# Optimization experiments

Measured on AMD Instinct MI355X. Metric: run time of the kernel, lower is better.

Reference implementation:

```python
import jax, jax.numpy as jnp
import numpy as np

NUM_EXPERTS = 8
DIM = 2048
BATCH = 8192


def setup_inputs() -> dict:
    key = jax.random.key(0)
    k_x, k_ids, k_w, k_b = jax.random.split(key, 4)
    x = jax.random.normal(k_x, (BATCH, DIM), dtype=jnp.float32)
    cam_pred_ids = jax.random.randint(k_ids, (BATCH,), 0, NUM_EXPERTS, dtype=jnp.int64)
    # torch nn.Linear default init: U(-1/sqrt(in), 1/sqrt(in)); W is [out, in]
    bound = 1.0 / np.sqrt(DIM)
    W = jax.random.uniform(k_w, (NUM_EXPERTS, DIM, DIM), dtype=jnp.float32,
                           minval=-bound, maxval=bound)
    b = jax.random.uniform(k_b, (NUM_EXPERTS, DIM), dtype=jnp.float32,
                           minval=-bound, maxval=bound)
    return {"x": x, "cam_pred_ids": cam_pred_ids, "W": W, "b": b}


def reference(x, cam_pred_ids, W, b):
    # Per-sample expert routing: out[i] = x[i] + relu(x[i] @ W[e].T + b[e]),
    # where e = cam_pred_ids[i]. Vectorized as 8 full-batch GEMMs with masked
    # combine (fixed small expert count -> Python loop is structural, not data).
    h = jnp.zeros_like(x)
    for e in range(NUM_EXPERTS):
        he = jax.nn.relu(x @ W[e].T + b[e])          # [B, D]
        mask = (cam_pred_ids == e)[:, None]
        h = h + jnp.where(mask, he, jnp.zeros((), dtype=x.dtype))
    return x + h
```

## Files before the change

### kernel.cpp

```cpp
#include <hip/hip_runtime.h>
#include <hip/hip_bf16.h>
#include <stdint.h>

#define BATCH 8192
#define DIM   2048
#define NEXP  8
#define BM    128
#define BN    128
#define BK    32
#define NITER (DIM / BK)
#define MAX_TILES 72
#define NBLK  (DIM / BN)
#define NROWS 9216
#define NCVTB 4096

typedef __bf16 bf16x8 __attribute__((ext_vector_type(8)));
typedef float  f32x4  __attribute__((ext_vector_type(4)));

#define XG_BYTE_OFF 40960ull
#define WB_BYTE_OFF 37789696ull
#define WS_NEED     104898560ull

#define AS1(p) ((const __attribute__((address_space(1))) void*)(p))
#define AS3(p) ((__attribute__((address_space(3))) void*)(p))

__device__ __forceinline__ unsigned f2bf2(float lo, float hi) {
    unsigned ul = __float_as_uint(lo), uh = __float_as_uint(hi);
    ul = (ul + 0x7FFFu + ((ul >> 16) & 1u)) >> 16;
    uh = (uh + 0x7FFFu + ((uh >> 16) & 1u)) >> 16;
    return (uh << 16) | ul;
}

__global__ void k_plan(const int* __restrict__ ids, int* __restrict__ ws,
                       int* __restrict__ rowmap) {
    __shared__ int sc[256 * NEXP];
    __shared__ int seg[NEXP];
    __shared__ int tot[NEXP];
    int t = threadIdx.x;
#pragma unroll
    for (int e = 0; e < NEXP; e++) sc[t * NEXP + e] = 0;
    int base = t * 32;
    for (int i = 0; i < 32; i++) sc[t * NEXP + ids[base + i]]++;
    __syncthreads();
    if (t < NEXP) {
        int run = 0;
        for (int j = 0; j < 256; j++) {
            int v = sc[j * NEXP + t];
            sc[j * NEXP + t] = run;
            run += v;
        }
        tot[t] = run;
    }
    __syncthreads();
    if (t == 0) {
        int pos = 0, mt = 0;
        for (int e = 0; e < NEXP; e++) {
            int c = tot[e];
            seg[e]     = pos;
            ws[e]      = c;
            ws[32 + e] = pos;
            int ntl = (c + BM - 1) / BM;
            for (int tt = 0; tt < ntl; tt++) {
                ws[64  + mt] = e;
                ws[160 + mt] = pos + tt * BM;
                int v = c - tt * BM;
                ws[256 + mt] = v < BM ? v : BM;
                mt++;
            }
            pos += ntl * BM;
        }
        ws[48] = mt;
        ws[49] = pos;
    }
    __syncthreads();
    for (int i = t; i < NROWS; i += 256) rowmap[i] = -1;
    __syncthreads();
    for (int i = 0; i < 32; i++) {
        int e = ids[base + i];
        int p = seg[e] + sc[t * NEXP + e]++;
        rowmap[p] = base + i;
    }
}

__global__ void k_prep(const float* __restrict__ x,
                       const int* __restrict__ rowmap,
                       unsigned short* __restrict__ xg,
                       const float4* __restrict__ W, uint4* __restrict__ Wb) {
    int b = blockIdx.x;
    int t = threadIdx.x;
    if (b >= NROWS) {
        size_t base = (size_t)(b - NROWS) * 1024;
#pragma unroll
        for (int j = 0; j < 4; j++) {
            size_t o = base + (size_t)j * 256 + t;
            float4 a = W[o * 2], c = W[o * 2 + 1];
            uint4 v;
            v.x = f2bf2(a.x, a.y);  v.y = f2bf2(a.z, a.w);
            v.z = f2bf2(c.x, c.y);  v.w = f2bf2(c.z, c.w);
            Wb[o] = v;
        }
        return;
    }
    int orig = rowmap[b];
    uint4* o = (uint4*)(xg + (size_t)b * DIM);
    if (orig < 0) {
        o[t] = make_uint4(0, 0, 0, 0);
        return;
    }
    const float4* xr = (const float4*)(x + (size_t)orig * DIM);
    float4 a = xr[t * 2], b4 = xr[t * 2 + 1];
    uint4 v;
    v.x = f2bf2(a.x, a.y);   v.y = f2bf2(a.z, a.w);
    v.z = f2bf2(b4.x, b4.y); v.w = f2bf2(b4.z, b4.w);
    o[t] = v;
}

__launch_bounds__(256)
__global__ void k_gemm(const unsigned short* __restrict__ xg,
                       const unsigned short* __restrict__ Wb,
                       const float* __restrict__ bias,
                       const int* __restrict__ ws, const int* __restrict__ rowmap,
                       float* __restrict__ out) {
    int bid = blockIdx.x;
    int g = bid >> 3, r = bid & 7;
    int nb = g & 15;
    int mt = ((g >> 4) << 3) + r;
    if (mt >= ws[48]) return;
    int e     = ws[64  + mt];
    int pos0  = ws[160 + mt];
    int valid = ws[256 + mt];
    int n0 = nb * BN;

    __shared__ unsigned short lds[2][8192];

    int tid = threadIdx.x;
    int w = tid >> 6, l = tid & 63;
    int lane15 = l & 15, quad = l >> 4;
    int wave_m = (w >> 1) * 64, wave_n = (w & 1) * 64;

    const unsigned short* Abase = xg + (size_t)pos0 * DIM;
    const unsigned short* Bbase = Wb + (size_t)e * DIM * DIM + (size_t)n0 * DIM;

    int srcOff[2];
#pragma unroll
    for (int j = 0; j < 2; j++) {
        int c = w * 128 + j * 64 + l;
        int row = c >> 2, pos = c & 3;
        int q = pos ^ ((row >> 1) & 3);
        srcOff[j] = row * DIM + q * 8;
    }

    int swz = (quad ^ ((lane15 >> 1) & 3)) * 8;
    int afOff[4], bfOff[4];
#pragma unroll
    for (int mi = 0; mi < 4; mi++)
        afOff[mi] = (wave_m + mi * 16 + lane15) * BK + swz;
#pragma unroll
    for (int ni = 0; ni < 4; ni++)
        bfOff[ni] = 4096 + (wave_n + ni * 16 + lane15) * BK + swz;

    f32x4 acc[4][4];
#pragma unroll
    for (int i = 0; i < 4; i++)
#pragma unroll
        for (int j = 0; j < 4; j++) acc[i][j] = (f32x4){0.f, 0.f, 0.f, 0.f};

#define ISSUE(buf, k0)                                                          \
    do {                                                                        \
        _Pragma("unroll")                                                       \
        for (int j = 0; j < 2; j++) {                                           \
            __builtin_amdgcn_global_load_lds(                                   \
                AS1(Abase + (k0) + srcOff[j]),                                  \
                AS3(&lds[buf][w * 1024 + j * 512]), 16, 0, 0);                  \
            __builtin_amdgcn_global_load_lds(                                   \
                AS1(Bbase + (k0) + srcOff[j]),                                  \
                AS3(&lds[buf][4096 + w * 1024 + j * 512]), 16, 0, 0);           \
        }                                                                       \
    } while (0)

    ISSUE(0, 0);
    int cur = 0;
    for (int i = 0; i < NITER; ++i) {
        __syncthreads();
        if (i + 1 < NITER) {
            int k0n = (i + 1) * BK;
            ISSUE(cur ^ 1, k0n);
        }
        bf16x8 af[4], bf[4];
#pragma unroll
        for (int mi = 0; mi < 4; mi++)
            af[mi] = *(const bf16x8*)(&lds[cur][afOff[mi]]);
#pragma unroll
        for (int ni = 0; ni < 4; ni++)
            bf[ni] = *(const bf16x8*)(&lds[cur][bfOff[ni]]);
#pragma unroll
        for (int mi = 0; mi < 4; mi++)
#pragma unroll
            for (int ni = 0; ni < 4; ni++)
                acc[mi][ni] = __builtin_amdgcn_mfma_f32_16x16x32_bf16(
                    af[mi], bf[ni], acc[mi][ni], 0, 0, 0);
        cur ^= 1;
    }
#undef ISSUE

    float bv[4];
#pragma unroll
    for (int ni = 0; ni < 4; ni++)
        bv[ni] = bias[(size_t)e * DIM + n0 + wave_n + ni * 16 + lane15];
#pragma unroll
    for (int mi = 0; mi < 4; mi++) {
#pragma unroll
        for (int r4 = 0; r4 < 4; r4++) {
            int rl = wave_m + mi * 16 + quad * 4 + r4;
            if (rl < valid) {
                int orig = rowmap[pos0 + rl];
                const unsigned short* xrow = xg + (size_t)(pos0 + rl) * DIM + n0;
                float* orow = out + (size_t)orig * DIM + n0;
#pragma unroll
                for (int ni = 0; ni < 4; ni++) {
                    int col = wave_n + ni * 16 + lane15;
                    float xv = __uint_as_float((unsigned)xrow[col] << 16);
                    float v = acc[mi][ni][r4] + bv[ni];
                    v = v > 0.f ? v : 0.f;
                    orow[col] = xv + v;
                }
            }
        }
    }
}

__global__ void k_naive(const float* __restrict__ x, const int* __restrict__ ids,
                        const float* __restrict__ W, const float* __restrict__ b,
                        float* __restrict__ out) {
    __shared__ float lx[DIM];
    int i = blockIdx.x;
    for (int t = threadIdx.x; t < DIM; t += blockDim.x) lx[t] = x[(size_t)i * DIM + t];
    __syncthreads();
    int e = ids[i];
    const float* We = W + (size_t)e * DIM * DIM;
    for (int n = threadIdx.x; n < DIM; n += blockDim.x) {
        const float* wr = We + (size_t)n * DIM;
        float acc = 0.f;
        for (int k = 0; k < DIM; k += 4) {
            float4 w4 = *(const float4*)(wr + k);
            acc += lx[k] * w4.x + lx[k + 1] * w4.y + lx[k + 2] * w4.z + lx[k + 3] * w4.w;
        }
        float v = acc + b[(size_t)e * DIM + n];
        v = v > 0.f ? v : 0.f;
        out[(size_t)i * DIM + n] = lx[n] + v;
    }
}

extern "C" void kernel_launch(void* const* d_in, const int* in_sizes, int n_in,
                              void* d_out, int out_size, void* d_ws, size_t ws_size,
                              hipStream_t stream) {
    const float* x   = (const float*)d_in[0];
    const int*   ids = (const int*)d_in[1];
    const float* W   = (const float*)d_in[2];
    const float* b   = (const float*)d_in[3];
    float* out = (float*)d_out;

    if (ws_size < WS_NEED) {
        k_naive<<<BATCH, 256, 0, stream>>>(x, ids, W, b, out);
        return;
    }

    char* wsb = (char*)d_ws;
    int*  wsi = (int*)wsb;
    unsigned short* xg = (unsigned short*)(wsb + XG_BYTE_OFF);
    unsigned short* Wb = (unsigned short*)(wsb + WB_BYTE_OFF);
    int* rowmap = wsi + 512;

    k_plan<<<1, 256, 0, stream>>>(ids, wsi, rowmap);
    k_prep<<<NROWS + NCVTB, 256, 0, stream>>>(x, rowmap, xg,
                                              (const float4*)W, (uint4*)Wb);
    k_gemm<<<NBLK * MAX_TILES, 256, 0, stream>>>(xg, Wb, b, wsi, rowmap, out);
}
```

Baseline: 403.0 us.

## Fuse activation gather and bf16 conversion into GEMM, merge plan into prep

Removes the separate gathered bf16 copy of x. The GEMM now loads fp32 rows of x through rowmap, converts them to bf16 in registers and writes them into swizzled LDS, while the weights still arrive by direct global-to-LDS loads. The planning kernel is folded into block 0 of the weight-conversion kernel and uses a wave-shuffle prefix scan, which saves a launch and a 9216-row staging pass. The residual now reads the original fp32 x. The trade-offs are register-path A loads inside the main loop, each row's activations being reconverted by all 16 N-blocks, and a block-index order that no longer groups tiles for L2 reuse.

```diff
diff --git a/kernel.cpp b/kernel.cpp
--- a/kernel.cpp
+++ b/kernel.cpp
@@ -11,13 +11,11 @@
 #define NITER (DIM / BK)
 #define MAX_TILES 72
 #define NBLK  (DIM / BN)
-#define NROWS 9216
 #define NCVTB 4096
 
 typedef __bf16 bf16x8 __attribute__((ext_vector_type(8)));
 typedef float  f32x4  __attribute__((ext_vector_type(4)));
 
-#define XG_BYTE_OFF 40960ull
 #define WB_BYTE_OFF 37789696ull
 #define WS_NEED     104898560ull
 
@@ -31,34 +29,60 @@
     return (uh << 16) | ul;
 }
 
-__global__ void k_plan(const int* __restrict__ ids, int* __restrict__ ws,
-                       int* __restrict__ rowmap) {
-    __shared__ int sc[256 * NEXP];
+__global__ __launch_bounds__(512)
+void k_prep(const int* __restrict__ ids, int* __restrict__ ws,
+            int* __restrict__ rowmap,
+            const float4* __restrict__ W, uint4* __restrict__ Wb) {
+    int b = blockIdx.x;
+    int t = threadIdx.x;
+    if (b > 0) {
+        size_t base = (size_t)(b - 1) * 1024;
+#pragma unroll
+        for (int j = 0; j < 2; j++) {
+            size_t o = base + (size_t)j * 512 + t;
+            float4 a = W[o * 2], c = W[o * 2 + 1];
+            uint4 v;
+            v.x = f2bf2(a.x, a.y);  v.y = f2bf2(a.z, a.w);
+            v.z = f2bf2(c.x, c.y);  v.w = f2bf2(c.z, c.w);
+            Wb[o] = v;
+        }
+        return;
+    }
+    __shared__ int sc[512 * NEXP];
     __shared__ int seg[NEXP];
     __shared__ int tot[NEXP];
-    int t = threadIdx.x;
+    int myids[16];
+    int base = t * 16;
 #pragma unroll
     for (int e = 0; e < NEXP; e++) sc[t * NEXP + e] = 0;
-    int base = t * 32;
-    for (int i = 0; i < 32; i++) sc[t * NEXP + ids[base + i]]++;
-    __syncthreads();
-    if (t < NEXP) {
-        int run = 0;
-        for (int j = 0; j < 256; j++) {
-            int v = sc[j * NEXP + t];
-            sc[j * NEXP + t] = run;
-            run += v;
-        }
-        tot[t] = run;
+#pragma unroll
+    for (int i = 0; i < 16; i++) {
+        myids[i] = ids[base + i];
+        sc[t * NEXP + myids[i]]++;
+    }
+    __syncthreads();
+    {
+        int w = t >> 6, l = t & 63;
+        int e = w;
+        int vals[8], sum = 0;
+#pragma unroll
+        for (int j = 0; j < 8; j++) { vals[j] = sc[(l * 8 + j) * NEXP + e]; sum += vals[j]; }
+        int inc = sum;
+        for (int d = 1; d < 64; d <<= 1) {
+            int v = __shfl_up(inc, d, 64);
+            if (l >= d) inc += v;
+        }
+        int run = inc - sum;
+#pragma unroll
+        for (int j = 0; j < 8; j++) { int v = vals[j]; sc[(l * 8 + j) * NEXP + e] = run; run += v; }
+        if (l == 63) tot[e] = run;
     }
     __syncthreads();
     if (t == 0) {
         int pos = 0, mt = 0;
         for (int e = 0; e < NEXP; e++) {
             int c = tot[e];
-            seg[e]     = pos;
-            ws[e]      = c;
-            ws[32 + e] = pos;
+            seg[e] = pos;
             int ntl = (c + BM - 1) / BM;
             for (int tt = 0; tt < ntl; tt++) {
                 ws[64  + mt] = e;
@@ -70,61 +94,24 @@
             pos += ntl * BM;
         }
         ws[48] = mt;
-        ws[49] = pos;
-    }
-    __syncthreads();
-    for (int i = t; i < NROWS; i += 256) rowmap[i] = -1;
-    __syncthreads();
-    for (int i = 0; i < 32; i++) {
-        int e = ids[base + i];
+    }
+    __syncthreads();
+#pragma unroll
+    for (int i = 0; i < 16; i++) {
+        int e = myids[i];
         int p = seg[e] + sc[t * NEXP + e]++;
         rowmap[p] = base + i;
     }
 }
 
-__global__ void k_prep(const float* __restrict__ x,
-                       const int* __restrict__ rowmap,
-                       unsigned short* __restrict__ xg,
-                       const float4* __restrict__ W, uint4* __restrict__ Wb) {
-    int b = blockIdx.x;
-    int t = threadIdx.x;
-    if (b >= NROWS) {
-        size_t base = (size_t)(b - NROWS) * 1024;
-#pragma unroll
-        for (int j = 0; j < 4; j++) {
-            size_t o = base + (size_t)j * 256 + t;
-            float4 a = W[o * 2], c = W[o * 2 + 1];
-            uint4 v;
-            v.x = f2bf2(a.x, a.y);  v.y = f2bf2(a.z, a.w);
-            v.z = f2bf2(c.x, c.y);  v.w = f2bf2(c.z, c.w);
-            Wb[o] = v;
-        }
-        return;
-    }
-    int orig = rowmap[b];
-    uint4* o = (uint4*)(xg + (size_t)b * DIM);
-    if (orig < 0) {
-        o[t] = make_uint4(0, 0, 0, 0);
-        return;
-    }
-    const float4* xr = (const float4*)(x + (size_t)orig * DIM);
-    float4 a = xr[t * 2], b4 = xr[t * 2 + 1];
-    uint4 v;
-    v.x = f2bf2(a.x, a.y);   v.y = f2bf2(a.z, a.w);
-    v.z = f2bf2(b4.x, b4.y); v.w = f2bf2(b4.z, b4.w);
-    o[t] = v;
-}
-
 __launch_bounds__(256)
-__global__ void k_gemm(const unsigned short* __restrict__ xg,
+__global__ void k_gemm(const float* __restrict__ x,
                        const unsigned short* __restrict__ Wb,
                        const float* __restrict__ bias,
                        const int* __restrict__ ws, const int* __restrict__ rowmap,
                        float* __restrict__ out) {
-    int bid = blockIdx.x;
-    int g = bid >> 3, r = bid & 7;
-    int nb = g & 15;
-    int mt = ((g >> 4) << 3) + r;
+    int nb = blockIdx.x;
+    int mt = blockIdx.y;
     if (mt >= ws[48]) return;
     int e     = ws[64  + mt];
     int pos0  = ws[160 + mt];
@@ -138,8 +125,17 @@
     int lane15 = l & 15, quad = l >> 4;
     int wave_m = (w >> 1) * 64, wave_n = (w & 1) * 64;
 
-    const unsigned short* Abase = xg + (size_t)pos0 * DIM;
     const unsigned short* Bbase = Wb + (size_t)e * DIM * DIM + (size_t)n0 * DIM;
+
+    int arow  = w * 32 + (l >> 1);
+    int ahalf = l & 1;
+    int s_r = (arow >> 1) & 3;
+    int aw0 = arow * BK + (((ahalf * 2)    ) ^ s_r) * 8;
+    int aw1 = arow * BK + (((ahalf * 2) + 1) ^ s_r) * 8;
+    bool aval = arow < valid;
+    const float4* asrc = nullptr;
+    if (aval)
+        asrc = (const float4*)(x + (size_t)rowmap[pos0 + arow] * DIM + ahalf * 16);
 
     int srcOff[2];
 #pragma unroll
@@ -165,26 +161,47 @@
 #pragma unroll
         for (int j = 0; j < 4; j++) acc[i][j] = (f32x4){0.f, 0.f, 0.f, 0.f};
 
-#define ISSUE(buf, k0)                                                          \
+#define ISSUE_B(buf, k0)                                                        \
     do {                                                                        \
         _Pragma("unroll")                                                       \
         for (int j = 0; j < 2; j++) {                                           \
-            __builtin_amdgcn_global_load_lds(                                   \
-                AS1(Abase + (k0) + srcOff[j]),                                  \
-                AS3(&lds[buf][w * 1024 + j * 512]), 16, 0, 0);                  \
             __builtin_amdgcn_global_load_lds(                                   \
                 AS1(Bbase + (k0) + srcOff[j]),                                  \
                 AS3(&lds[buf][4096 + w * 1024 + j * 512]), 16, 0, 0);           \
         }                                                                       \
     } while (0)
 
-    ISSUE(0, 0);
+#define CVT_WRITE(buf, a0, a1, a2, a3)                                          \
+    do {                                                                        \
+        bf16x8 c0, c1;                                                          \
+        c0[0] = (__bf16)a0.x; c0[1] = (__bf16)a0.y;                             \
+        c0[2] = (__bf16)a0.z; c0[3] = (__bf16)a0.w;                             \
+        c0[4] = (__bf16)a1.x; c0[5] = (__bf16)a1.y;                             \
+        c0[6] = (__bf16)a1.z; c0[7] = (__bf16)a1.w;                             \
+        c1[0] = (__bf16)a2.x; c1[1] = (__bf16)a2.y;                             \
+        c1[2] = (__bf16)a2.z; c1[3] = (__bf16)a2.w;                             \
+        c1[4] = (__bf16)a3.x; c1[5] = (__bf16)a3.y;                             \
+        c1[6] = (__bf16)a3.z; c1[7] = (__bf16)a3.w;                             \
+        *(bf16x8*)(&lds[buf][aw0]) = c0;                                        \
+        *(bf16x8*)(&lds[buf][aw1]) = c1;                                        \
+    } while (0)
+
+    {
+        float4 a0 = {0,0,0,0}, a1 = {0,0,0,0}, a2 = {0,0,0,0}, a3 = {0,0,0,0};
+        if (aval) { a0 = asrc[0]; a1 = asrc[1]; a2 = asrc[2]; a3 = asrc[3]; }
+        CVT_WRITE(0, a0, a1, a2, a3);
+        ISSUE_B(0, 0);
+    }
     int cur = 0;
     for (int i = 0; i < NITER; ++i) {
         __syncthreads();
+        float4 a0 = {0,0,0,0}, a1 = {0,0,0,0}, a2 = {0,0,0,0}, a3 = {0,0,0,0};
         if (i + 1 < NITER) {
-            int k0n = (i + 1) * BK;
-            ISSUE(cur ^ 1, k0n);
+            if (aval) {
+                const float4* p = asrc + (i + 1) * (BK / 4);
+                a0 = p[0]; a1 = p[1]; a2 = p[2]; a3 = p[3];
+            }
+            ISSUE_B(cur ^ 1, (i + 1) * BK);
         }
         bf16x8 af[4], bf[4];
 #pragma unroll
@@ -199,9 +216,12 @@
             for (int ni = 0; ni < 4; ni++)
                 acc[mi][ni] = __builtin_amdgcn_mfma_f32_16x16x32_bf16(
                     af[mi], bf[ni], acc[mi][ni], 0, 0, 0);
+        if (i + 1 < NITER)
+            CVT_WRITE(cur ^ 1, a0, a1, a2, a3);
         cur ^= 1;
     }
-#undef ISSUE
+#undef ISSUE_B
+#undef CVT_WRITE
 
     float bv[4];
 #pragma unroll
@@ -214,15 +234,14 @@
             int rl = wave_m + mi * 16 + quad * 4 + r4;
             if (rl < valid) {
                 int orig = rowmap[pos0 + rl];
-                const unsigned short* xrow = xg + (size_t)(pos0 + rl) * DIM + n0;
+                const float* xrow = x + (size_t)orig * DIM + n0;
                 float* orow = out + (size_t)orig * DIM + n0;
 #pragma unroll
                 for (int ni = 0; ni < 4; ni++) {
                     int col = wave_n + ni * 16 + lane15;
-                    float xv = __uint_as_float((unsigned)xrow[col] << 16);
                     float v = acc[mi][ni][r4] + bv[ni];
                     v = v > 0.f ? v : 0.f;
-                    orow[col] = xv + v;
+                    orow[col] = xrow[col] + v;
                 }
             }
         }
@@ -267,12 +286,11 @@
 
     char* wsb = (char*)d_ws;
     int*  wsi = (int*)wsb;
-    unsigned short* xg = (unsigned short*)(wsb + XG_BYTE_OFF);
     unsigned short* Wb = (unsigned short*)(wsb + WB_BYTE_OFF);
     int* rowmap = wsi + 512;
 
-    k_plan<<<1, 256, 0, stream>>>(ids, wsi, rowmap);
-    k_prep<<<NROWS + NCVTB, 256, 0, stream>>>(x, rowmap, xg,
-                                              (const float4*)W, (uint4*)Wb);
-    k_gemm<<<NBLK * MAX_TILES, 256, 0, stream>>>(xg, Wb, b, wsi, rowmap, out);
-}
+    k_prep<<<NCVTB + 1, 512, 0, stream>>>(ids, wsi, rowmap,
+                                          (const float4*)W, (uint4*)Wb);
+    dim3 g(NBLK, MAX_TILES);
+    k_gemm<<<g, 256, 0, stream>>>(x, Wb, b, wsi, rowmap, out);
+}
```

After: 431.6 us. +7.1%, slower.
